# Optimization experiments

Hardware: AMD Instinct MI355X
Metric: run time of the kernel (lower is better)

The kernel has to match this reference:

```python
import jax, jax.numpy as jnp
import numpy as np

B, W, H, V, L = 64, 512, 1024, 32000, 2


def setup_inputs() -> dict:
    key = jax.random.key(0)
    ks = jax.random.split(key, 20)
    s = 0.02  # init scale
    n = lambda k, shp: jax.random.normal(k, shp, jnp.float32)
    return {
        "input": jax.random.randint(ks[0], (B, 1), 0, V),
        "h0": n(ks[1], (L, B, H)),
        "c0": n(ks[2], (L, B, H)),
        "encoder_output": n(ks[3], (B, W, H)),
        "embedding": n(ks[4], (V, H)) * s,
        "W_ih0": n(ks[5], (4 * H, H)) * s,
        "W_hh0": n(ks[6], (4 * H, H)) * s,
        "b_ih0": n(ks[7], (4 * H,)) * s,
        "b_hh0": n(ks[8], (4 * H,)) * s,
        "W_ih1": n(ks[9], (4 * H, H)) * s,
        "W_hh1": n(ks[10], (4 * H, H)) * s,
        "b_ih1": n(ks[11], (4 * H,)) * s,
        "b_hh1": n(ks[12], (4 * H,)) * s,
        "att_w": n(ks[13], (2 * H,)) * s,
        "att_b": n(ks[14], (1,)) * s,
        "input_W": n(ks[15], (H, 2 * H)) * s,
        "input_b": n(ks[16], (H,)) * s,
        "out_W": n(ks[17], (V, H)) * s,
        "out_b": n(ks[18], (V,)) * s,
    }


def _lstm_step(x, h, c, W_ih, W_hh, b_ih, b_hh):
    # PyTorch gate order: i, f, g, o
    g = x @ W_ih.T + h @ W_hh.T + b_ih + b_hh
    i, f, gg, o = jnp.split(g, 4, axis=-1)
    c2 = jax.nn.sigmoid(f) * c + jax.nn.sigmoid(i) * jnp.tanh(gg)
    return jax.nn.sigmoid(o) * jnp.tanh(c2), c2


def reference(input, h0, c0, encoder_output, embedding,
              W_ih0, W_hh0, b_ih0, b_hh0, W_ih1, W_hh1, b_ih1, b_hh1,
              att_w, att_b, input_W, input_b, out_W, out_b):
    Hd = h0.shape[-1]
    emb = embedding[input]                       # (B,1,H)
    att_state = h0[-1] * c0[-1]                  # (B,H)
    # Vectorized replacement of the per-word cat+linear loop:
    # att_line(cat(enc_w, att_state)) = enc_w @ w_enc + att_state @ w_st + b
    w_enc, w_st = att_w[:Hd], att_w[Hd:]
    scores = encoder_output @ w_enc + (att_state @ w_st)[:, None] + att_b[0]  # (B,W)
    # Original quirk: weigth starts with a zeros column, then softmax over
    # weigth[:, 0:-1] -> zero column + scores for words 0..W-2 (last dropped).
    zeros = jnp.zeros((scores.shape[0], 1), scores.dtype)
    full = jnp.concatenate([zeros, scores[:, :-1]], axis=1)  # (B,W)
    wts = jax.nn.softmax(full, axis=1)
    ctx = jnp.einsum('bw,bwh->bh', wts, encoder_output)      # (B,H)
    x = jnp.concatenate([ctx, emb[:, 0, :]], axis=-1)        # (B,2H)
    x = x @ input_W.T + input_b                              # (B,H)
    h1, c1 = _lstm_step(x, h0[0], c0[0], W_ih0, W_hh0, b_ih0, b_hh0)
    h2, c2 = _lstm_step(h1, h0[1], c0[1], W_ih1, W_hh1, b_ih1, b_hh1)
    logits = h2 @ out_W.T + out_b                            # (B,V)
    logp = jax.nn.log_softmax(logits, axis=-1)[:, None, :]   # (B,1,V)
    return logp, jnp.stack([h1, h2]), jnp.stack([c1, c2])
```

## Files before the change

### kernel.cpp

```cpp
#include <hip/hip_runtime.h>
#include <hip/hip_bf16.h>

#define Bsz 64
#define Wln 512
#define Hd  1024
#define Vc  32000

typedef short v8s __attribute__((ext_vector_type(8)));
typedef float f32x4 __attribute__((ext_vector_type(4)));

__device__ inline unsigned short f2b(float f) {
  union { float f; unsigned u; } v; v.f = f;
  return (unsigned short)((v.u + 0x8000u) >> 16);
}
__device__ inline float wave_sum(float v) {
  #pragma unroll
  for (int o = 32; o; o >>= 1) v += __shfl_down(v, o);
  return v;
}
__device__ inline float wave_max(float v) {
  #pragma unroll
  for (int o = 32; o; o >>= 1) v = fmaxf(v, __shfl_down(v, o));
  return v;
}
__device__ inline float sigm(float x) { return 1.f / (1.f + expf(-x)); }

__device__ inline v8s cvt_frag(float4 x0, float4 x1) {
  v8s r;
  r[0] = (short)f2b(x0.x); r[1] = (short)f2b(x0.y);
  r[2] = (short)f2b(x0.z); r[3] = (short)f2b(x0.w);
  r[4] = (short)f2b(x1.x); r[5] = (short)f2b(x1.y);
  r[6] = (short)f2b(x1.z); r[7] = (short)f2b(x1.w);
  return r;
}

__global__ __launch_bounds__(256) void k_scores_satt(
    const float* __restrict__ enc, const float* __restrict__ att_w,
    const float* __restrict__ h0, const float* __restrict__ c0,
    const float* __restrict__ att_b, const int* __restrict__ input,
    const float* __restrict__ emb,
    float* __restrict__ scores, float* __restrict__ s_att,
    float* __restrict__ cat)
{
  __shared__ float red[4];
  int t = threadIdx.x;
  if (blockIdx.x < 8192) {
    int row = blockIdx.x * 4 + (t >> 6);
    int lane = t & 63;
    const float* p = enc + (size_t)row * Hd + lane * 16;
    const float* w = att_w + lane * 16;
    float s = 0.f;
    #pragma unroll
    for (int c = 0; c < 4; ++c) {
      float4 e = *(const float4*)(p + c * 4);
      float4 ww = *(const float4*)(w + c * 4);
      s += e.x * ww.x + e.y * ww.y + e.z * ww.z + e.w * ww.w;
    }
    s = wave_sum(s);
    if (lane == 0) scores[row] = s;
  } else {
    int b = blockIdx.x - 8192;
    int idx = input[b];
    for (int j = t; j < Hd; j += 256)
      cat[b * 2 * Hd + Hd + j] = emb[(size_t)idx * Hd + j];
    size_t base = (size_t)(Bsz + b) * Hd;
    float s = 0.f;
    for (int j = t; j < Hd; j += 256)
      s += h0[base + j] * c0[base + j] * att_w[Hd + j];
    s = wave_sum(s);
    if ((t & 63) == 0) red[t >> 6] = s;
    __syncthreads();
    if (t == 0) s_att[b] = red[0] + red[1] + red[2] + red[3] + att_b[0];
  }
}

__global__ __launch_bounds__(256) void k_ctx_part(
    const float* __restrict__ scores, const float* __restrict__ s_att,
    const float* __restrict__ enc, float* __restrict__ part)
{
  int b = blockIdx.x >> 3, ch = blockIdx.x & 7;
  int t = threadIdx.x;
  float sa = s_att[b];
  const float* sr = scores + b * Wln;
  int w0 = t * 2, w1 = t * 2 + 1;
  float v0 = (w0 == 0) ? 0.f : sr[w0 - 1] + sa;
  float v1 = sr[w1 - 1] + sa;
  __shared__ float redm[4], reds[4];
  float m = fmaxf(v0, v1);
  m = wave_max(m);
  if ((t & 63) == 0) redm[t >> 6] = m;
  __syncthreads();
  float M = fmaxf(fmaxf(redm[0], redm[1]), fmaxf(redm[2], redm[3]));
  float e = expf(v0 - M) + expf(v1 - M);
  e = wave_sum(e);
  if ((t & 63) == 0) reds[t >> 6] = e;
  __syncthreads();
  float S = reds[0] + reds[1] + reds[2] + reds[3];
  __shared__ float w[64];
  if (t < 64) {
    int wg = ch * 64 + t;
    float v = (wg == 0) ? 0.f : sr[wg - 1] + sa;
    w[t] = expf(v - M) / S;
  }
  __syncthreads();
  int h4 = t * 4;
  const float* p = enc + (size_t)b * Wln * Hd + (size_t)ch * 64 * Hd + h4;
  float a0 = 0, a1 = 0, a2 = 0, a3 = 0;
  #pragma unroll 4
  for (int i = 0; i < 64; ++i) {
    float4 ev = *(const float4*)(p + (size_t)i * Hd);
    float wi = w[i];
    a0 += wi * ev.x; a1 += wi * ev.y; a2 += wi * ev.z; a3 += wi * ev.w;
  }
  float* o = part + ((size_t)b * 8 + ch) * Hd + h4;
  o[0] = a0; o[1] = a1; o[2] = a2; o[3] = a3;
}

__global__ __launch_bounds__(256) void k_ctx_red(
    const float* __restrict__ part, float* __restrict__ cat)
{
  int idx = blockIdx.x * 256 + threadIdx.x;
  int b = idx >> 10, h = idx & 1023;
  float s = 0.f;
  #pragma unroll
  for (int c = 0; c < 8; ++c) s += part[((size_t)b * 8 + c) * Hd + h];
  cat[b * 2 * Hd + h] = s;
}

template<int NS>
__global__ __launch_bounds__(512, 2) void gemm_v6(
    const float* __restrict__ A1, const float* __restrict__ A1b, int sA1,
    const float* __restrict__ B1, int sB1, const float* __restrict__ bias1,
    float* __restrict__ out1,
    const float* __restrict__ A2, const float* __restrict__ A2b, int sA2,
    const float* __restrict__ B2, int sB2, const float* __restrict__ bias2,
    float* __restrict__ out2,
    int N, int nblk1)
{
  constexpr int KS  = 8 / NS;
  constexpr int KSL = 1024 / KS;
  constexpr int NCH = KSL / 32;
  const int tid = threadIdx.x;

  const float *A, *Ab, *B, *bias; float* out; int sA, sB, bid;
  if ((int)blockIdx.x < nblk1) {
    A = A1; Ab = A1b; sA = sA1; B = B1; sB = sB1; bias = bias1; out = out1;
    bid = blockIdx.x;
  } else {
    A = A2; Ab = A2b; sA = sA2; B = B2; sB = sB2; bias = bias2; out = out2;
    bid = blockIdx.x - nblk1;
  }

  __shared__ __align__(16) char pool[131072];

  const int w = tid >> 6, lane = tid & 63;
  const int r = lane & 15, q = lane >> 4;
  const int nsub = w % NS, kh = w / NS;
  const int n0 = bid * (NS * 16);

  const float* bp = B + (size_t)(n0 + nsub * 16 + r) * sB + kh * KSL + q * 8;
  float4 breg[NCH][2];
  #pragma unroll
  for (int kk = 0; kk < NCH; ++kk) {
    breg[kk][0] = *(const float4*)(bp + kk * 32);
    breg[kk][1] = *(const float4*)(bp + kk * 32 + 4);
  }

  #pragma unroll
  for (int it = 0; it < 16; ++it) {
    int idx = it * 512 + tid;
    int row = idx >> 7, ch = idx & 127;
    const float* src = A + (size_t)row * sA + ch * 8;
    float4 x0 = *(const float4*)src;
    float4 x1 = *(const float4*)(src + 4);
    if (Ab) {
      const float* s2 = Ab + (size_t)row * sA + ch * 8;
      float4 y0 = *(const float4*)s2;
      float4 y1 = *(const float4*)(s2 + 4);
      x0.x += y0.x; x0.y += y0.y; x0.z += y0.z; x0.w += y0.w;
      x1.x += y1.x; x1.y += y1.y; x1.z += y1.z; x1.w += y1.w;
    }
    *(v8s*)(pool + row * 2048 + ((ch * 16) ^ ((row & 7) << 4))) = cvt_frag(x0, x1);
  }
  __syncthreads();

  f32x4 acc[4] = {{0,0,0,0},{0,0,0,0},{0,0,0,0},{0,0,0,0}};
  const int swz = (r & 7) << 4;

  #pragma unroll
  for (int kk = 0; kk < NCH; ++kk) {
    v8s bf = cvt_frag(breg[kk][0], breg[kk][1]);
    int cb = ((kh * KSL + kk * 32 + q * 8) * 2) ^ swz;
    #pragma unroll
    for (int m = 0; m < 4; ++m) {
      v8s af = *(const v8s*)(pool + (m * 16 + r) * 2048 + cb);
      acc[m] = __builtin_amdgcn_mfma_f32_16x16x32_bf16(af, bf, acc[m], 0, 0, 0);
    }
  }

  __syncthreads();
  float (*red)[64][17] = (float(*)[64][17])pool;
  #pragma unroll
  for (int m = 0; m < 4; ++m)
    #pragma unroll
    for (int rr = 0; rr < 4; ++rr)
      red[w][lane][m * 4 + rr] = acc[m][rr];
  __syncthreads();

  constexpr int COLS = NS * 16;
  #pragma unroll
  for (int it = 0; it < NS * 2; ++it) {
    int e = it * 512 + tid;
    int cc = e % COLS, rowi = e / COLS;
    int ns2 = cc >> 4, lo = cc & 15;
    int idx = ((rowi >> 4) << 2) + (rowi & 3);
    int le  = (((rowi >> 2) & 3) << 4) + lo;
    float s = 0.f;
    #pragma unroll
    for (int j = 0; j < KS; ++j) s += red[ns2 + j * NS][le][idx];
    float bb = bias ? bias[n0 + cc] : 0.f;
    out[(size_t)rowi * N + n0 + cc] = s + bb;
  }
}

__global__ __launch_bounds__(256) void k_lstm(
    const float* __restrict__ g1, const float* __restrict__ g2,
    const float* __restrict__ c0,
    float* __restrict__ out_h, float* __restrict__ out_c)
{
  int b = blockIdx.x >> 2;
  int j = ((blockIdx.x & 3) << 8) + threadIdx.x;
  const float* ga = g1 + (size_t)b * 4 * Hd;
  const float* gb = g2 + (size_t)b * 4 * Hd;
  float gi = ga[j] + gb[j];
  float gf = ga[Hd + j] + gb[Hd + j];
  float gg = ga[2 * Hd + j] + gb[2 * Hd + j];
  float go = ga[3 * Hd + j] + gb[3 * Hd + j];
  float c = sigm(gf) * c0[(size_t)b * Hd + j] + sigm(gi) * tanhf(gg);
  float h = sigm(go) * tanhf(c);
  out_h[b * Hd + j] = h;
  out_c[b * Hd + j] = c;
}

__global__ __launch_bounds__(1024) void k_logsoftmax(float* __restrict__ lg)
{
  int b = blockIdx.x, t = threadIdx.x;
  float* row = lg + (size_t)b * Vc;
  __shared__ float red[16];
  float m = -1e30f;
  for (int w = t * 4; w < Vc; w += 4096) {
    float4 v = *(const float4*)(row + w);
    m = fmaxf(m, fmaxf(fmaxf(v.x, v.y), fmaxf(v.z, v.w)));
  }
  m = wave_max(m);
  if ((t & 63) == 0) red[t >> 6] = m;
  __syncthreads();
  float M = red[0];
  #pragma unroll
  for (int i = 1; i < 16; ++i) M = fmaxf(M, red[i]);
  __syncthreads();
  float s = 0.f;
  for (int w = t * 4; w < Vc; w += 4096) {
    float4 v = *(const float4*)(row + w);
    s += expf(v.x - M) + expf(v.y - M) + expf(v.z - M) + expf(v.w - M);
  }
  s = wave_sum(s);
  if ((t & 63) == 0) red[t >> 6] = s;
  __syncthreads();
  float S = red[0];
  #pragma unroll
  for (int i = 1; i < 16; ++i) S += red[i];
  float lse = M + logf(S);
  for (int w = t * 4; w < Vc; w += 4096) {
    float4 v = *(const float4*)(row + w);
    v.x -= lse; v.y -= lse; v.z -= lse; v.w -= lse;
    *(float4*)(row + w) = v;
  }
}

extern "C" void kernel_launch(void* const* d_in, const int* in_sizes, int n_in,
                              void* d_out, int out_size, void* d_ws, size_t ws_size,
                              hipStream_t stream)
{
  const int*   input = (const int*)d_in[0];
  const float* h0    = (const float*)d_in[1];
  const float* c0    = (const float*)d_in[2];
  const float* enc   = (const float*)d_in[3];
  const float* emb   = (const float*)d_in[4];
  const float* W_ih0 = (const float*)d_in[5];
  const float* W_hh0 = (const float*)d_in[6];
  const float* b_ih0 = (const float*)d_in[7];
  const float* b_hh0 = (const float*)d_in[8];
  const float* W_ih1 = (const float*)d_in[9];
  const float* W_hh1 = (const float*)d_in[10];
  const float* b_ih1 = (const float*)d_in[11];
  const float* b_hh1 = (const float*)d_in[12];
  const float* att_w = (const float*)d_in[13];
  const float* att_b = (const float*)d_in[14];
  const float* inW   = (const float*)d_in[15];
  const float* inb   = (const float*)d_in[16];
  const float* outW  = (const float*)d_in[17];
  const float* outb  = (const float*)d_in[18];
  float* out = (float*)d_out;

  char* sc = (char*)d_out;
  float* g1     = (float*)(sc + 0);
  float* g2     = (float*)(sc + 1048576);
  float* ctxp   = (float*)(sc + 2097152);
  float* cat    = (float*)(sc + 4194304);
  float* x1     = (float*)(sc + 4718592);
  float* x2     = (float*)(sc + 4980736);
  float* scores = (float*)(sc + 5242880);
  float* s_att  = (float*)(sc + 5505024);

  float* out_h = out + (size_t)Bsz * Vc;
  float* out_c = out_h + 2 * Bsz * Hd;
  float* h1 = out_h;
  float* h2 = out_h + Bsz * Hd;

  k_scores_satt<<<8256, 256, 0, stream>>>(enc, att_w, h0, c0, att_b, input, emb,
                                          scores, s_att, cat);
  k_ctx_part<<<Bsz * 8, 256, 0, stream>>>(scores, s_att, enc, ctxp);
  k_ctx_red<<<Bsz * Hd / 256, 256, 0, stream>>>(ctxp, cat);

  gemm_v6<1><<<128, 512, 0, stream>>>(
      cat,      nullptr, 2 * Hd, inW,      2 * Hd, inb,     x1,
      cat + Hd, nullptr, 2 * Hd, inW + Hd, 2 * Hd, nullptr, x2,
      Hd, 64);

  gemm_v6<2><<<256, 512, 0, stream>>>(
      x1, x2,      Hd, W_ih0, Hd, b_ih0, g1,
      h0, nullptr, Hd, W_hh0, Hd, b_hh0, g2,
      4 * Hd, 128);
  k_lstm<<<Bsz * 4, 256, 0, stream>>>(g1, g2, c0, h1, out_c);

  gemm_v6<2><<<256, 512, 0, stream>>>(
      h1,                     nullptr, Hd, W_ih1, Hd, b_ih1, g1,
      h0 + (size_t)Bsz * Hd,  nullptr, Hd, W_hh1, Hd, b_hh1, g2,
      4 * Hd, 128);
  k_lstm<<<Bsz * 4, 256, 0, stream>>>(g1, g2, c0 + (size_t)Bsz * Hd, h2, out_c + Bsz * Hd);

  gemm_v6<4><<<500, 512, 0, stream>>>(
      h2,      nullptr, Hd, outW,    Hd, outb,    out,
      nullptr, nullptr, 0,  nullptr, 0,  nullptr, nullptr,
      Vc, 500);
  k_logsoftmax<<<Bsz, 1024, 0, stream>>>(out);
}
```

Before: 149.2 us.

## Fuse context reduction, input GEMM halves, gate GEMMs with LSTM, and split log-softmax

Rebuilds most of the pipeline. The context partial and reduce kernels merge into one block-level kernel. The two input-projection halves are accumulated in a single GEMM instead of being summed later. The ih and hh gate GEMMs are fused with the LSTM cell using an interleaved gate column mapping, which removes the g1/g2 intermediates and the separate LSTM kernels. Log-softmax is split across four blocks per row with a partial max/sum pass, and scratch moves from the output buffer to the workspace. The cost is more K-serial work per block in the fused GEMMs and fewer blocks (64 and 128), which may reduce parallelism.

```diff
diff --git a/kernel.cpp b/kernel.cpp
--- a/kernel.cpp
+++ b/kernel.cpp
@@ -32,6 +32,19 @@
   r[4] = (short)f2b(x1.x); r[5] = (short)f2b(x1.y);
   r[6] = (short)f2b(x1.z); r[7] = (short)f2b(x1.w);
   return r;
+}
+
+__device__ inline void stage_A(const float* __restrict__ A, int sA,
+                               char* pool, int tid) {
+  #pragma unroll
+  for (int it = 0; it < 16; ++it) {
+    int idx = it * 512 + tid;
+    int row = idx >> 7, ch = idx & 127;
+    const float* src = A + (size_t)row * sA + ch * 8;
+    float4 x0 = *(const float4*)src;
+    float4 x1 = *(const float4*)(src + 4);
+    *(v8s*)(pool + row * 2048 + ((ch * 16) ^ ((row & 7) << 4))) = cvt_frag(x0, x1);
+  }
 }
 
 __global__ __launch_bounds__(256) void k_scores_satt(
@@ -74,131 +87,219 @@
   }
 }
 
-__global__ __launch_bounds__(256) void k_ctx_part(
+__global__ __launch_bounds__(512) void k_ctx(
     const float* __restrict__ scores, const float* __restrict__ s_att,
-    const float* __restrict__ enc, float* __restrict__ part)
-{
-  int b = blockIdx.x >> 3, ch = blockIdx.x & 7;
-  int t = threadIdx.x;
+    const float* __restrict__ enc, float* __restrict__ cat)
+{
+  __shared__ float w_sh[Wln];
+  __shared__ float part[8][256];
+  __shared__ float redA[8], redB[8];
+  int b = blockIdx.x >> 2, qtr = blockIdx.x & 3;
+  int tid = threadIdx.x, w = tid >> 6, lane = tid & 63;
   float sa = s_att[b];
   const float* sr = scores + b * Wln;
-  int w0 = t * 2, w1 = t * 2 + 1;
-  float v0 = (w0 == 0) ? 0.f : sr[w0 - 1] + sa;
-  float v1 = sr[w1 - 1] + sa;
-  __shared__ float redm[4], reds[4];
-  float m = fmaxf(v0, v1);
-  m = wave_max(m);
-  if ((t & 63) == 0) redm[t >> 6] = m;
-  __syncthreads();
-  float M = fmaxf(fmaxf(redm[0], redm[1]), fmaxf(redm[2], redm[3]));
-  float e = expf(v0 - M) + expf(v1 - M);
-  e = wave_sum(e);
-  if ((t & 63) == 0) reds[t >> 6] = e;
-  __syncthreads();
-  float S = reds[0] + reds[1] + reds[2] + reds[3];
-  __shared__ float w[64];
-  if (t < 64) {
-    int wg = ch * 64 + t;
-    float v = (wg == 0) ? 0.f : sr[wg - 1] + sa;
-    w[t] = expf(v - M) / S;
-  }
-  __syncthreads();
-  int h4 = t * 4;
-  const float* p = enc + (size_t)b * Wln * Hd + (size_t)ch * 64 * Hd + h4;
+  float v = (tid == 0) ? 0.f : sr[tid - 1] + sa;
+  float m = wave_max(v);
+  if (lane == 0) redA[w] = m;
+  __syncthreads();
+  float M = redA[0];
+  #pragma unroll
+  for (int i = 1; i < 8; ++i) M = fmaxf(M, redA[i]);
+  float e = expf(v - M);
+  float s = wave_sum(e);
+  if (lane == 0) redB[w] = s;
+  __syncthreads();
+  float S = redB[0];
+  #pragma unroll
+  for (int i = 1; i < 8; ++i) S += redB[i];
+  w_sh[tid] = e / S;
+  __syncthreads();
+
+  const float* pb = enc + (size_t)b * Wln * Hd + qtr * 256 + lane * 4;
   float a0 = 0, a1 = 0, a2 = 0, a3 = 0;
   #pragma unroll 4
   for (int i = 0; i < 64; ++i) {
-    float4 ev = *(const float4*)(p + (size_t)i * Hd);
-    float wi = w[i];
+    int row = w * 64 + i;
+    float4 ev = *(const float4*)(pb + (size_t)row * Hd);
+    float wi = w_sh[row];
     a0 += wi * ev.x; a1 += wi * ev.y; a2 += wi * ev.z; a3 += wi * ev.w;
   }
-  float* o = part + ((size_t)b * 8 + ch) * Hd + h4;
-  o[0] = a0; o[1] = a1; o[2] = a2; o[3] = a3;
-}
-
-__global__ __launch_bounds__(256) void k_ctx_red(
-    const float* __restrict__ part, float* __restrict__ cat)
-{
-  int idx = blockIdx.x * 256 + threadIdx.x;
-  int b = idx >> 10, h = idx & 1023;
-  float s = 0.f;
-  #pragma unroll
-  for (int c = 0; c < 8; ++c) s += part[((size_t)b * 8 + c) * Hd + h];
-  cat[b * 2 * Hd + h] = s;
-}
-
-template<int NS>
-__global__ __launch_bounds__(512, 2) void gemm_v6(
-    const float* __restrict__ A1, const float* __restrict__ A1b, int sA1,
-    const float* __restrict__ B1, int sB1, const float* __restrict__ bias1,
-    float* __restrict__ out1,
-    const float* __restrict__ A2, const float* __restrict__ A2b, int sA2,
-    const float* __restrict__ B2, int sB2, const float* __restrict__ bias2,
-    float* __restrict__ out2,
-    int N, int nblk1)
-{
-  constexpr int KS  = 8 / NS;
-  constexpr int KSL = 1024 / KS;
-  constexpr int NCH = KSL / 32;
+  part[w][lane * 4 + 0] = a0; part[w][lane * 4 + 1] = a1;
+  part[w][lane * 4 + 2] = a2; part[w][lane * 4 + 3] = a3;
+  __syncthreads();
+  if (tid < 256) {
+    float s2 = 0.f;
+    #pragma unroll
+    for (int ww = 0; ww < 8; ++ww) s2 += part[ww][tid];
+    cat[b * 2 * Hd + qtr * 256 + tid] = s2;
+  }
+}
+
+__global__ __launch_bounds__(512) void k_input_gemm(
+    const float* __restrict__ cat, const float* __restrict__ inW,
+    const float* __restrict__ inb, float* __restrict__ x)
+{
+  __shared__ __align__(16) char pool[131072];
   const int tid = threadIdx.x;
-
-  const float *A, *Ab, *B, *bias; float* out; int sA, sB, bid;
-  if ((int)blockIdx.x < nblk1) {
-    A = A1; Ab = A1b; sA = sA1; B = B1; sB = sB1; bias = bias1; out = out1;
-    bid = blockIdx.x;
-  } else {
-    A = A2; Ab = A2b; sA = sA2; B = B2; sB = sB2; bias = bias2; out = out2;
-    bid = blockIdx.x - nblk1;
-  }
-
-  __shared__ __align__(16) char pool[131072];
-
   const int w = tid >> 6, lane = tid & 63;
   const int r = lane & 15, q = lane >> 4;
-  const int nsub = w % NS, kh = w / NS;
-  const int n0 = bid * (NS * 16);
-
-  const float* bp = B + (size_t)(n0 + nsub * 16 + r) * sB + kh * KSL + q * 8;
-  float4 breg[NCH][2];
-  #pragma unroll
-  for (int kk = 0; kk < NCH; ++kk) {
+  const int kh = w;
+  const int n0 = blockIdx.x * 16;
+
+  f32x4 acc[4] = {{0,0,0,0},{0,0,0,0},{0,0,0,0},{0,0,0,0}};
+  #pragma unroll
+  for (int p = 0; p < 2; ++p) {
+    const float* bp = inW + (size_t)(n0 + r) * 2048 + p * 1024 + kh * 128 + q * 8;
+    float4 breg[4][2];
+    #pragma unroll
+    for (int kk = 0; kk < 4; ++kk) {
+      breg[kk][0] = *(const float4*)(bp + kk * 32);
+      breg[kk][1] = *(const float4*)(bp + kk * 32 + 4);
+    }
+    stage_A(cat + p * 1024, 2048, pool, tid);
+    __syncthreads();
+    const int swz = (r & 7) << 4;
+    #pragma unroll
+    for (int kk = 0; kk < 4; ++kk) {
+      v8s bf = cvt_frag(breg[kk][0], breg[kk][1]);
+      int cb = ((kh * 128 + kk * 32 + q * 8) * 2) ^ swz;
+      #pragma unroll
+      for (int m = 0; m < 4; ++m) {
+        v8s af = *(const v8s*)(pool + (m * 16 + r) * 2048 + cb);
+        acc[m] = __builtin_amdgcn_mfma_f32_16x16x32_bf16(af, bf, acc[m], 0, 0, 0);
+      }
+    }
+    __syncthreads();
+  }
+
+  float (*red)[64][17] = (float(*)[64][17])pool;
+  #pragma unroll
+  for (int m = 0; m < 4; ++m)
+    #pragma unroll
+    for (int rr = 0; rr < 4; ++rr)
+      red[w][lane][m * 4 + rr] = acc[m][rr];
+  __syncthreads();
+
+  #pragma unroll
+  for (int it = 0; it < 2; ++it) {
+    int e = it * 512 + tid;
+    int cc = e & 15, rowi = e >> 4;
+    int idx = ((rowi >> 4) << 2) + (rowi & 3);
+    int le  = (((rowi >> 2) & 3) << 4) + cc;
+    float s = 0.f;
+    #pragma unroll
+    for (int j = 0; j < 8; ++j) s += red[j][le][idx];
+    x[(size_t)rowi * Hd + n0 + cc] = s + inb[n0 + cc];
+  }
+}
+
+__global__ __launch_bounds__(512) void k_gate_lstm(
+    const float* __restrict__ xA, const float* __restrict__ hA,
+    const float* __restrict__ W_ih, const float* __restrict__ W_hh,
+    const float* __restrict__ b_ih, const float* __restrict__ b_hh,
+    const float* __restrict__ c0,
+    float* __restrict__ out_h, float* __restrict__ out_c)
+{
+  __shared__ __align__(16) char pool[131072];
+  const int tid = threadIdx.x;
+  const int w = tid >> 6, lane = tid & 63;
+  const int r = lane & 15, q = lane >> 4;
+  const int nsub = w & 1, kh = w >> 1;
+  const int cc_w = nsub * 16 + r;
+  const int gate = cc_w >> 3, jl = cc_w & 7;
+  const size_t Brow = (size_t)(gate * Hd + blockIdx.x * 8 + jl);
+
+  f32x4 acc[4] = {{0,0,0,0},{0,0,0,0},{0,0,0,0},{0,0,0,0}};
+  const float* Amat[2] = { xA, hA };
+  const float* Wmat[2] = { W_ih, W_hh };
+  #pragma unroll
+  for (int p = 0; p < 2; ++p) {
+    const float* bp = Wmat[p] + Brow * Hd + kh * 256 + q * 8;
+    float4 breg[8][2];
+    #pragma unroll
+    for (int kk = 0; kk < 8; ++kk) {
+      breg[kk][0] = *(const float4*)(bp + kk * 32);
+      breg[kk][1] = *(const float4*)(bp + kk * 32 + 4);
+    }
+    stage_A(Amat[p], Hd, pool, tid);
+    __syncthreads();
+    const int swz = (r & 7) << 4;
+    #pragma unroll
+    for (int kk = 0; kk < 8; ++kk) {
+      v8s bf = cvt_frag(breg[kk][0], breg[kk][1]);
+      int cb = ((kh * 256 + kk * 32 + q * 8) * 2) ^ swz;
+      #pragma unroll
+      for (int m = 0; m < 4; ++m) {
+        v8s af = *(const v8s*)(pool + (m * 16 + r) * 2048 + cb);
+        acc[m] = __builtin_amdgcn_mfma_f32_16x16x32_bf16(af, bf, acc[m], 0, 0, 0);
+      }
+    }
+    __syncthreads();
+  }
+
+  float (*red)[64][17] = (float(*)[64][17])pool;
+  #pragma unroll
+  for (int m = 0; m < 4; ++m)
+    #pragma unroll
+    for (int rr = 0; rr < 4; ++rr)
+      red[w][lane][m * 4 + rr] = acc[m][rr];
+  __syncthreads();
+
+  int b = tid >> 3, jl2 = tid & 7;
+  int jg = blockIdx.x * 8 + jl2;
+  float gv[4];
+  #pragma unroll
+  for (int g2 = 0; g2 < 4; ++g2) {
+    int cc = g2 * 8 + jl2;
+    int ns2 = cc >> 4, lo = cc & 15;
+    int idx = ((b >> 4) << 2) + (b & 3);
+    int le  = (((b >> 2) & 3) << 4) + lo;
+    float s = 0.f;
+    #pragma unroll
+    for (int j = 0; j < 4; ++j) s += red[ns2 + j * 2][le][idx];
+    gv[g2] = s + b_ih[g2 * Hd + jg] + b_hh[g2 * Hd + jg];
+  }
+  float c = sigm(gv[1]) * c0[(size_t)b * Hd + jg] + sigm(gv[0]) * tanhf(gv[2]);
+  float h = sigm(gv[3]) * tanhf(c);
+  out_h[(size_t)b * Hd + jg] = h;
+  out_c[(size_t)b * Hd + jg] = c;
+}
+
+__global__ __launch_bounds__(512) void k_logits(
+    const float* __restrict__ A, const float* __restrict__ B,
+    const float* __restrict__ bias, float* __restrict__ out)
+{
+  __shared__ __align__(16) char pool[131072];
+  const int tid = threadIdx.x;
+  const int w = tid >> 6, lane = tid & 63;
+  const int r = lane & 15, q = lane >> 4;
+  const int nsub = w & 3, kh = w >> 2;
+  const int n0 = blockIdx.x * 64;
+
+  const float* bp = B + (size_t)(n0 + nsub * 16 + r) * Hd + kh * 512 + q * 8;
+  float4 breg[16][2];
+  #pragma unroll
+  for (int kk = 0; kk < 16; ++kk) {
     breg[kk][0] = *(const float4*)(bp + kk * 32);
     breg[kk][1] = *(const float4*)(bp + kk * 32 + 4);
   }
-
-  #pragma unroll
-  for (int it = 0; it < 16; ++it) {
-    int idx = it * 512 + tid;
-    int row = idx >> 7, ch = idx & 127;
-    const float* src = A + (size_t)row * sA + ch * 8;
-    float4 x0 = *(const float4*)src;
-    float4 x1 = *(const float4*)(src + 4);
-    if (Ab) {
-      const float* s2 = Ab + (size_t)row * sA + ch * 8;
-      float4 y0 = *(const float4*)s2;
-      float4 y1 = *(const float4*)(s2 + 4);
-      x0.x += y0.x; x0.y += y0.y; x0.z += y0.z; x0.w += y0.w;
-      x1.x += y1.x; x1.y += y1.y; x1.z += y1.z; x1.w += y1.w;
-    }
-    *(v8s*)(pool + row * 2048 + ((ch * 16) ^ ((row & 7) << 4))) = cvt_frag(x0, x1);
-  }
+  stage_A(A, Hd, pool, tid);
   __syncthreads();
 
   f32x4 acc[4] = {{0,0,0,0},{0,0,0,0},{0,0,0,0},{0,0,0,0}};
   const int swz = (r & 7) << 4;
-
-  #pragma unroll
-  for (int kk = 0; kk < NCH; ++kk) {
+  #pragma unroll
+  for (int kk = 0; kk < 16; ++kk) {
     v8s bf = cvt_frag(breg[kk][0], breg[kk][1]);
-    int cb = ((kh * KSL + kk * 32 + q * 8) * 2) ^ swz;
+    int cb = ((kh * 512 + kk * 32 + q * 8) * 2) ^ swz;
     #pragma unroll
     for (int m = 0; m < 4; ++m) {
       v8s af = *(const v8s*)(pool + (m * 16 + r) * 2048 + cb);
       acc[m] = __builtin_amdgcn_mfma_f32_16x16x32_bf16(af, bf, acc[m], 0, 0, 0);
     }
   }
-
-  __syncthreads();
+  __syncthreads();
+
   float (*red)[64][17] = (float(*)[64][17])pool;
   #pragma unroll
   for (int m = 0; m < 4; ++m)
@@ -207,74 +308,69 @@
       red[w][lane][m * 4 + rr] = acc[m][rr];
   __syncthreads();
 
-  constexpr int COLS = NS * 16;
-  #pragma unroll
-  for (int it = 0; it < NS * 2; ++it) {
+  #pragma unroll
+  for (int it = 0; it < 8; ++it) {
     int e = it * 512 + tid;
-    int cc = e % COLS, rowi = e / COLS;
+    int cc = e & 63, rowi = e >> 6;
     int ns2 = cc >> 4, lo = cc & 15;
     int idx = ((rowi >> 4) << 2) + (rowi & 3);
     int le  = (((rowi >> 2) & 3) << 4) + lo;
-    float s = 0.f;
-    #pragma unroll
-    for (int j = 0; j < KS; ++j) s += red[ns2 + j * NS][le][idx];
-    float bb = bias ? bias[n0 + cc] : 0.f;
-    out[(size_t)rowi * N + n0 + cc] = s + bb;
-  }
-}
-
-__global__ __launch_bounds__(256) void k_lstm(
-    const float* __restrict__ g1, const float* __restrict__ g2,
-    const float* __restrict__ c0,
-    float* __restrict__ out_h, float* __restrict__ out_c)
-{
-  int b = blockIdx.x >> 2;
-  int j = ((blockIdx.x & 3) << 8) + threadIdx.x;
-  const float* ga = g1 + (size_t)b * 4 * Hd;
-  const float* gb = g2 + (size_t)b * 4 * Hd;
-  float gi = ga[j] + gb[j];
-  float gf = ga[Hd + j] + gb[Hd + j];
-  float gg = ga[2 * Hd + j] + gb[2 * Hd + j];
-  float go = ga[3 * Hd + j] + gb[3 * Hd + j];
-  float c = sigm(gf) * c0[(size_t)b * Hd + j] + sigm(gi) * tanhf(gg);
-  float h = sigm(go) * tanhf(c);
-  out_h[b * Hd + j] = h;
-  out_c[b * Hd + j] = c;
-}
-
-__global__ __launch_bounds__(1024) void k_logsoftmax(float* __restrict__ lg)
-{
-  int b = blockIdx.x, t = threadIdx.x;
-  float* row = lg + (size_t)b * Vc;
-  __shared__ float red[16];
+    float s = red[ns2][le][idx] + red[ns2 + 4][le][idx];
+    out[(size_t)rowi * Vc + n0 + cc] = s + bias[n0 + cc];
+  }
+}
+
+__global__ __launch_bounds__(512) void k_lsm_part(
+    const float* __restrict__ lg, float* __restrict__ pm, float* __restrict__ ps)
+{
+  __shared__ float redA[8], redB[8];
+  int b = blockIdx.x >> 2, qc = blockIdx.x & 3;
+  int tid = threadIdx.x, w = tid >> 6, lane = tid & 63;
+  const float* row = lg + (size_t)b * Vc + qc * 8000;
   float m = -1e30f;
-  for (int w = t * 4; w < Vc; w += 4096) {
-    float4 v = *(const float4*)(row + w);
+  for (int j = tid * 4; j < 8000; j += 2048) {
+    float4 v = *(const float4*)(row + j);
     m = fmaxf(m, fmaxf(fmaxf(v.x, v.y), fmaxf(v.z, v.w)));
   }
   m = wave_max(m);
-  if ((t & 63) == 0) red[t >> 6] = m;
-  __syncthreads();
-  float M = red[0];
-  #pragma unroll
-  for (int i = 1; i < 16; ++i) M = fmaxf(M, red[i]);
-  __syncthreads();
+  if (lane == 0) redA[w] = m;
+  __syncthreads();
+  float M = redA[0];
+  #pragma unroll
+  for (int i = 1; i < 8; ++i) M = fmaxf(M, redA[i]);
   float s = 0.f;
-  for (int w = t * 4; w < Vc; w += 4096) {
-    float4 v = *(const float4*)(row + w);
+  for (int j = tid * 4; j < 8000; j += 2048) {
+    float4 v = *(const float4*)(row + j);
     s += expf(v.x - M) + expf(v.y - M) + expf(v.z - M) + expf(v.w - M);
   }
   s = wave_sum(s);
-  if ((t & 63) == 0) red[t >> 6] = s;
-  __syncthreads();
-  float S = red[0];
-  #pragma unroll
-  for (int i = 1; i < 16; ++i) S += red[i];
+  if (lane == 0) redB[w] = s;
+  __syncthreads();
+  if (tid == 0) {
+    float S = redB[0];
+    #pragma unroll
+    for (int i = 1; i < 8; ++i) S += redB[i];
+    pm[blockIdx.x] = M; ps[blockIdx.x] = S;
+  }
+}
+
+__global__ __launch_bounds__(512) void k_lsm_sub(
+    float* __restrict__ lg, const float* __restrict__ pm, const float* __restrict__ ps)
+{
+  int b = blockIdx.x >> 2, qc = blockIdx.x & 3;
+  int tid = threadIdx.x;
+  float M = pm[b * 4];
+  #pragma unroll
+  for (int i = 1; i < 4; ++i) M = fmaxf(M, pm[b * 4 + i]);
+  float S = 0.f;
+  #pragma unroll
+  for (int i = 0; i < 4; ++i) S += ps[b * 4 + i] * expf(pm[b * 4 + i] - M);
   float lse = M + logf(S);
-  for (int w = t * 4; w < Vc; w += 4096) {
-    float4 v = *(const float4*)(row + w);
+  float* row = lg + (size_t)b * Vc + qc * 8000;
+  for (int j = tid * 4; j < 8000; j += 2048) {
+    float4 v = *(const float4*)(row + j);
     v.x -= lse; v.y -= lse; v.z -= lse; v.w -= lse;
-    *(float4*)(row + w) = v;
+    *(float4*)(row + j) = v;
   }
 }
 
@@ -303,15 +399,13 @@
   const float* outb  = (const float*)d_in[18];
   float* out = (float*)d_out;
 
-  char* sc = (char*)d_out;
-  float* g1     = (float*)(sc + 0);
-  float* g2     = (float*)(sc + 1048576);
-  float* ctxp   = (float*)(sc + 2097152);
-  float* cat    = (float*)(sc + 4194304);
-  float* x1     = (float*)(sc + 4718592);
-  float* x2     = (float*)(sc + 4980736);
-  float* scores = (float*)(sc + 5242880);
-  float* s_att  = (float*)(sc + 5505024);
+  char* ws = (char*)d_ws;
+  float* cat    = (float*)(ws + 0);
+  float* x      = (float*)(ws + 524288);
+  float* scores = (float*)(ws + 786432);
+  float* s_att  = (float*)(ws + 917504);
+  float* pm     = (float*)(ws + 918528);
+  float* ps     = (float*)(ws + 919552);
 
   float* out_h = out + (size_t)Bsz * Vc;
   float* out_c = out_h + 2 * Bsz * Hd;
@@ -320,29 +414,14 @@
 
   k_scores_satt<<<8256, 256, 0, stream>>>(enc, att_w, h0, c0, att_b, input, emb,
                                           scores, s_att, cat);
-  k_ctx_part<<<Bsz * 8, 256, 0, stream>>>(scores, s_att, enc, ctxp);
-  k_ctx_red<<<Bsz * Hd / 256, 256, 0, stream>>>(ctxp, cat);
-
-  gemm_v6<1><<<128, 512, 0, stream>>>(
-      cat,      nullptr, 2 * Hd, inW,      2 * Hd, inb,     x1,
-      cat + Hd, nullptr, 2 * Hd, inW + Hd, 2 * Hd, nullptr, x2,
-      Hd, 64);
-
-  gemm_v6<2><<<256, 512, 0, stream>>>(
-      x1, x2,      Hd, W_ih0, Hd, b_ih0, g1,
-      h0, nullptr, Hd, W_hh0, Hd, b_hh0, g2,
-      4 * Hd, 128);
-  k_lstm<<<Bsz * 4, 256, 0, stream>>>(g1, g2, c0, h1, out_c);
-
-  gemm_v6<2><<<256, 512, 0, stream>>>(
-      h1,                     nullptr, Hd, W_ih1, Hd, b_ih1, g1,
-      h0 + (size_t)Bsz * Hd,  nullptr, Hd, W_hh1, Hd, b_hh1, g2,
-      4 * Hd, 128);
-  k_lstm<<<Bsz * 4, 256, 0, stream>>>(g1, g2, c0 + (size_t)Bsz * Hd, h2, out_c + Bsz * Hd);
-
-  gemm_v6<4><<<500, 512, 0, stream>>>(
-      h2,      nullptr, Hd, outW,    Hd, outb,    out,
-      nullptr, nullptr, 0,  nullptr, 0,  nullptr, nullptr,
-      Vc, 500);
-  k_logsoftmax<<<Bsz, 1024, 0, stream>>>(out);
-}
+  k_ctx<<<Bsz * 4, 512, 0, stream>>>(scores, s_att, enc, cat);
+  k_input_gemm<<<64, 512, 0, stream>>>(cat, inW, inb, x);
+  k_gate_lstm<<<128, 512, 0, stream>>>(x, h0, W_ih0, W_hh0, b_ih0, b_hh0,
+                                       c0, h1, out_c);
+  k_gate_lstm<<<128, 512, 0, stream>>>(h1, h0 + (size_t)Bsz * Hd, W_ih1, W_hh1,
+                                       b_ih1, b_hh1, c0 + (size_t)Bsz * Hd,
+                                       h2, out_c + Bsz * Hd);
+  k_logits<<<500, 512, 0, stream>>>(h2, outW, outb, out);
+  k_lsm_part<<<256, 512, 0, stream>>>(out, pm, ps);
+  k_lsm_sub<<<256, 512, 0, stream>>>(out, pm, ps);
+}
```

New measurement: 142.3 us. -4.6%, faster.
